# Performance work log

Measured on AMD Instinct MI355X. Metric: run time of the kernel, lower is better.

Reference implementation:

```python
import jax, jax.numpy as jnp
import numpy as np
import math

D_MODEL = 512
N_HEADS = 8
D_K = D_MODEL // N_HEADS
B, N = 2, 2048


def setup_inputs() -> dict:
    key = jax.random.key(0)
    ks = jax.random.split(key, 13)
    s = 1.0 / math.sqrt(D_MODEL)
    inp = {
        "x": jax.random.normal(ks[0], (B, N, D_MODEL), dtype=jnp.float32),
        "D": jax.random.uniform(ks[1], (B, N, N), dtype=jnp.float32),
        "A": jax.random.uniform(ks[2], (B, N, N), dtype=jnp.float32),
        "Wq": jax.random.normal(ks[3], (D_MODEL, D_MODEL), dtype=jnp.float32) * s,
        "bq": jnp.zeros((D_MODEL,), dtype=jnp.float32),
        "Wk": jax.random.normal(ks[4], (D_MODEL, D_MODEL), dtype=jnp.float32) * s,
        "bk": jnp.zeros((D_MODEL,), dtype=jnp.float32),
        "Wv": jax.random.normal(ks[5], (D_MODEL, D_MODEL), dtype=jnp.float32) * s,
        "bv": jnp.zeros((D_MODEL,), dtype=jnp.float32),
        "Wo": jax.random.normal(ks[6], (D_MODEL, D_MODEL), dtype=jnp.float32) * s,
        "bo": jnp.zeros((D_MODEL,), dtype=jnp.float32),
        # learned per-head bias scalars; init nonzero so biases matter numerically
        "w_d": jax.random.normal(ks[7], (1, N_HEADS, 1, 1), dtype=jnp.float32) * 0.1,
        "w_a": jax.random.normal(ks[8], (1, N_HEADS, 1, 1), dtype=jnp.float32) * 0.1,
    }
    return inp


def reference(x, D, A, Wq, bq, Wk, bk, Wv, bv, Wo, bo, w_d, w_a):
    b, n, _ = x.shape
    # project and split heads: (B, H, N, d_k)
    def heads(W, bias):
        return (x @ W.T + bias).reshape(b, n, N_HEADS, D_K).transpose(0, 2, 1, 3)
    q = heads(Wq, bq)
    k = heads(Wk, bk)
    v = heads(Wv, bv)
    scale = 1.0 / math.sqrt(D_K)
    # (B, H, N, N) scores with learned-scalar-weighted tree biases
    scores = jnp.einsum("bhqd,bhkd->bhqk", q, k) * scale
    scores = scores + w_d * D[:, None, :, :] + w_a * A[:, None, :, :]
    attn = jax.nn.softmax(scores, axis=-1)
    out = jnp.einsum("bhqk,bhkd->bhqd", attn, v)
    out = out.transpose(0, 2, 1, 3).reshape(b, n, D_MODEL)
    return out @ Wo.T + bo
```

## Files before the change

kernel.cpp:

```cpp
#include <hip/hip_runtime.h>
#include <hip/hip_bf16.h>
#include <math.h>

typedef unsigned short ushort_t;
typedef unsigned int   uint_t;
typedef __attribute__((ext_vector_type(8))) short  bf16x8;
typedef __attribute__((ext_vector_type(4))) float  f32x4;
typedef __attribute__((ext_vector_type(2))) int    i32x2;
typedef __attribute__((ext_vector_type(4))) short  s16x4;

#define MFMA16(a, b, c) __builtin_amdgcn_mfma_f32_16x16x32_bf16((a), (b), (c), 0, 0, 0)

static constexpr int BATCH = 2;
static constexpr int SEQ   = 2048;
static constexpr int DMODEL = 512;
static constexpr int NHEADS = 8;
static constexpr int DK    = 64;
static constexpr int MROWS = BATCH * SEQ;
static constexpr int XE = MROWS * DMODEL;
static constexpr int WE = DMODEL * DMODEL;
static constexpr int NQKV = 3 * DMODEL;
static constexpr int NSPLIT = 4;
static constexpr int KB_PER = (SEQ / 64) / NSPLIT;

static constexpr float QSCALE_L2E = 0.18033688011112043f;
static constexpr float L2E = 1.4426950408889634f;

__device__ __forceinline__ ushort_t f2bf(float f) {
  unsigned int u = __builtin_bit_cast(unsigned int, f);
  u = (u + 0x7FFFu + ((u >> 16) & 1u)) >> 16;
  return (ushort_t)u;
}

__device__ __forceinline__ float fexp2(float x) {
  float r;
  asm("v_exp_f32 %0, %1" : "=v"(r) : "v"(x));
  return r;
}

__device__ __forceinline__ int cvt_pk_bf16(float a, float b) {
  int r;
  asm("v_cvt_pk_bf16_f32 %0, %1, %2" : "=v"(r) : "v"(a), "v"(b));
  return r;
}

__device__ __forceinline__ float rowmax16(float x) {
  int t;
  t = __builtin_amdgcn_mov_dpp(__builtin_bit_cast(int, x), 0xB1, 0xF, 0xF, true);
  x = fmaxf(x, __builtin_bit_cast(float, t));
  t = __builtin_amdgcn_mov_dpp(__builtin_bit_cast(int, x), 0x4E, 0xF, 0xF, true);
  x = fmaxf(x, __builtin_bit_cast(float, t));
  t = __builtin_amdgcn_mov_dpp(__builtin_bit_cast(int, x), 0x141, 0xF, 0xF, true);
  x = fmaxf(x, __builtin_bit_cast(float, t));
  t = __builtin_amdgcn_mov_dpp(__builtin_bit_cast(int, x), 0x140, 0xF, 0xF, true);
  x = fmaxf(x, __builtin_bit_cast(float, t));
  return x;
}

__device__ __forceinline__ void async16(const ushort_t* g, ushort_t* l) {
  __builtin_amdgcn_global_load_lds(
      (const __attribute__((address_space(1))) unsigned int*)g,
      (__attribute__((address_space(3))) unsigned int*)l, 16, 0, 0);
}

__global__ __launch_bounds__(256) void convert_kernel(
    const float* __restrict__ x,  const float* __restrict__ wq,
    const float* __restrict__ wk, const float* __restrict__ wv,
    const float* __restrict__ wo,
    const float* __restrict__ bq, const float* __restrict__ bk,
    const float* __restrict__ bv,
    ushort_t* __restrict__ dst, float* __restrict__ bqkv) {
  const int bid = blockIdx.x;
  if (bid == (XE + 4 * WE) / 1024) {
    for (int i = threadIdx.x; i < NQKV; i += 256) {
      bqkv[i] = (i < 512) ? bq[i] * QSCALE_L2E
              : (i < 1024) ? bk[i - 512] : bv[i - 1024];
    }
    return;
  }
  int e = (bid * 256 + threadIdx.x) * 4;
  const float* src;
  int off;
  float qs = 1.0f;
  if (e < XE)                { src = x;  off = e; }
  else if (e < XE + WE)      { src = wq; off = e - XE; qs = QSCALE_L2E; }
  else if (e < XE + 2 * WE)  { src = wk; off = e - XE - WE; }
  else if (e < XE + 3 * WE)  { src = wv; off = e - XE - 2 * WE; }
  else                       { src = wo; off = e - XE - 3 * WE; }
  float4 f = *reinterpret_cast<const float4*>(&src[off]);
  s16x4 v;
  v[0] = (short)f2bf(f.x * qs); v[1] = (short)f2bf(f.y * qs);
  v[2] = (short)f2bf(f.z * qs); v[3] = (short)f2bf(f.w * qs);
  *reinterpret_cast<s16x4*>(&dst[e]) = v;
}

template <bool F32OUT>
__global__ __launch_bounds__(256) void gemm_bt128(
    const ushort_t* __restrict__ A, const ushort_t* __restrict__ Bt,
    const float* __restrict__ bias, void* __restrict__ C,
    int N, int K) {
  __shared__ ushort_t As[128][64];
  __shared__ ushort_t Bs[128][64];
  const int tid  = threadIdx.x;
  const int wave = tid >> 6, lane = tid & 63;
  const int quad = lane >> 4, l15 = lane & 15;
  const int m0 = blockIdx.y * 128, n0 = blockIdx.x * 128;
  const int wr = (wave >> 1) * 64, wc = (wave & 1) * 64;

  f32x4 acc[4][4] = {};

  const int lrow = lane >> 3, slot = lane & 7;
  const int cswz = 8 * (slot ^ lrow);
  const ushort_t* ag = A  + (size_t)(m0 + wave * 8 + lrow) * K + cswz;
  const ushort_t* bg = Bt + (size_t)(n0 + wave * 8 + lrow) * K + cswz;
  ushort_t* la[4]; ushort_t* lb[4];
#pragma unroll
  for (int r0 = 0; r0 < 4; r0++) {
    la[r0] = &As[r0 * 32 + wave * 8][0];
    lb[r0] = &Bs[r0 * 32 + wave * 8][0];
  }

  const int swz = l15 & 7;

  for (int k0 = 0; k0 < K; k0 += 64) {
    __syncthreads();
#pragma unroll
    for (int r0 = 0; r0 < 4; r0++)
      async16(ag + k0 + (size_t)(r0 * 32) * K, la[r0]);
#pragma unroll
    for (int r0 = 0; r0 < 4; r0++)
      async16(bg + k0 + (size_t)(r0 * 32) * K, lb[r0]);
    asm volatile("s_waitcnt vmcnt(0)" ::: "memory");
    __syncthreads();
#pragma unroll
    for (int s = 0; s < 2; s++) {
      const int acol = 8 * ((s * 4 + quad) ^ swz);
      bf16x8 af[4], bfr[4];
#pragma unroll
      for (int i = 0; i < 4; i++)
        af[i] = *reinterpret_cast<const bf16x8*>(&As[wr + i * 16 + l15][acol]);
#pragma unroll
      for (int j = 0; j < 4; j++)
        bfr[j] = *reinterpret_cast<const bf16x8*>(&Bs[wc + j * 16 + l15][acol]);
#pragma unroll
      for (int i = 0; i < 4; i++)
#pragma unroll
        for (int j = 0; j < 4; j++)
          acc[i][j] = MFMA16(af[i], bfr[j], acc[i][j]);
    }
  }

#pragma unroll
  for (int j = 0; j < 4; j++) {
    const int col = n0 + wc + j * 16 + l15;
    const float bv = bias[col];
#pragma unroll
    for (int i = 0; i < 4; i++) {
#pragma unroll
      for (int rr = 0; rr < 4; rr++) {
        const int row = m0 + wr + i * 16 + quad * 4 + rr;
        const float v = acc[i][j][rr] + bv;
        if (F32OUT) reinterpret_cast<float*>(C)[(size_t)row * N + col] = v;
        else        reinterpret_cast<ushort_t*>(C)[(size_t)row * N + col] = f2bf(v);
      }
    }
  }
}

__global__ __launch_bounds__(256) void attn_kernel(
    const ushort_t* __restrict__ QKV,
    const float* __restrict__ Dm, const float* __restrict__ Am,
    const float* __restrict__ wd, const float* __restrict__ wa,
    float* __restrict__ Opart, float* __restrict__ Mp, float* __restrict__ Lp) {
  const int qb = blockIdx.x, h = blockIdx.y;
  const int b = blockIdx.z / NSPLIT, split = blockIdx.z % NSPLIT;
  const int tid = threadIdx.x;
  const int wave = tid >> 6, lane = tid & 63;
  const int quad = lane >> 4, l15 = lane & 15;
  const int q0 = qb * 64;
  const float wdh = wd[h] * L2E, wah = wa[h] * L2E;

  __shared__ ushort_t Ks[64][64];
  __shared__ ushort_t Vts[64][64];
  __shared__ __align__(16) ushort_t Ps[4][16][72];

  const int qrow = q0 + wave * 16 + l15;
  bf16x8 qf[2];
#pragma unroll
  for (int s = 0; s < 2; s++)
    qf[s] = *reinterpret_cast<const bf16x8*>(
        &QKV[(size_t)(b * SEQ + qrow) * NQKV + h * DK + s * 32 + quad * 8]);

  bf16x8 ones;
#pragma unroll
  for (int j = 0; j < 8; j++) ones[j] = (short)0x3F80;

  float m_run[4], l_run[4];
  f32x4 o[4] = {};
#pragma unroll
  for (int rr = 0; rr < 4; rr++) { m_run[rr] = -INFINITY; l_run[rr] = 0.f; }

  const int lrow = lane >> 3, slot = lane & 7;
  const ushort_t* kg = QKV + (size_t)(b * SEQ + wave * 16 + lrow) * NQKV +
                       512 + h * DK + 8 * (slot ^ lrow);
  ushort_t* lk0 = &Ks[wave * 16][0];
  ushort_t* lk1 = &Ks[wave * 16 + 8][0];

  const int u  = tid >> 3;
  const int c7 = tid & 7;
  const int sc = c7 * 8;
  const int kv = ((u & 3) << 4) | (u >> 2);
  const ushort_t* vg = QKV + (size_t)(b * SEQ + kv) * NQKV + 1024 + h * DK + sc;
  const int col0 = (u & 7) + 8 * ((u >> 3) ^ c7);
  const int col1 = (u & 7) + 8 * (((u >> 3) + 4) ^ c7);

  const int swz = l15 & 7;

  const float* dD[4];
  const float* dA[4];
#pragma unroll
  for (int rr = 0; rr < 4; rr++) {
    const size_t rowoff = (size_t)b * SEQ * SEQ +
        (size_t)(q0 + wave * 16 + quad * 4 + rr) * SEQ + (size_t)split * KB_PER * 64 + l15;
    dD[rr] = Dm + rowoff;
    dA[rr] = Am + rowoff;
  }

  for (int kbi = 0; kbi < KB_PER; kbi++) {
    const int k0 = (split * KB_PER + kbi) * 64;
    __syncthreads();
    async16(kg + (size_t)k0 * NQKV, lk0);
    async16(kg + (size_t)(k0 + 8) * NQKV, lk1);
    bf16x8 v0 = *reinterpret_cast<const bf16x8*>(vg + (size_t)k0 * NQKV);
    bf16x8 v1 = *reinterpret_cast<const bf16x8*>(vg + (size_t)(k0 + 8) * NQKV);

    float dv[4][4], av[4][4];
#pragma unroll
    for (int t = 0; t < 4; t++) {
#pragma unroll
      for (int rr = 0; rr < 4; rr++) {
        dv[t][rr] = dD[rr][t * 16];
        av[t][rr] = dA[rr][t * 16];
      }
    }
#pragma unroll
    for (int rr = 0; rr < 4; rr++) { dD[rr] += 64; dA[rr] += 64; }

#pragma unroll
    for (int j = 0; j < 8; j++) {
      Vts[sc + j][col0] = (ushort_t)v0[j];
      Vts[sc + j][col1] = (ushort_t)v1[j];
    }
    asm volatile("s_waitcnt vmcnt(0)" ::: "memory");
    __syncthreads();

    f32x4 sacc[4];
#pragma unroll
    for (int t = 0; t < 4; t++) {
      bf16x8 kf0 = *reinterpret_cast<const bf16x8*>(&Ks[t * 16 + l15][8 * (quad ^ swz)]);
      bf16x8 kf1 = *reinterpret_cast<const bf16x8*>(&Ks[t * 16 + l15][8 * ((4 + quad) ^ swz)]);
      f32x4 z = {};
      z = MFMA16(qf[0], kf0, z);
      sacc[t] = MFMA16(qf[1], kf1, z);
    }

    float sv[4][4];
    float mx[4] = {-INFINITY, -INFINITY, -INFINITY, -INFINITY};
#pragma unroll
    for (int t = 0; t < 4; t++) {
#pragma unroll
      for (int rr = 0; rr < 4; rr++) {
        float s = fmaf(wdh, dv[t][rr], fmaf(wah, av[t][rr], sacc[t][rr]));
        sv[t][rr] = s;
        mx[rr] = fmaxf(mx[rr], s);
      }
    }
#pragma unroll
    for (int rr = 0; rr < 4; rr++) mx[rr] = rowmax16(mx[rr]);

    bool grow = false;
#pragma unroll
    for (int rr = 0; rr < 4; rr++) grow |= (mx[rr] > m_run[rr] + 11.5f);
    if (__ballot(grow)) {
      float alpha[4];
#pragma unroll
      for (int rr = 0; rr < 4; rr++) {
        const float mn = fmaxf(m_run[rr], mx[rr]);
        alpha[rr] = fexp2(m_run[rr] - mn);
        m_run[rr] = mn;
        l_run[rr] *= alpha[rr];
      }
#pragma unroll
      for (int dt = 0; dt < 4; dt++)
#pragma unroll
        for (int rr = 0; rr < 4; rr++) o[dt][rr] *= alpha[rr];
    }

#pragma unroll
    for (int rr = 0; rr < 4; rr++) {
      const float m = m_run[rr];
      i32x2 w;
      w[0] = cvt_pk_bf16(fexp2(sv[0][rr] - m), fexp2(sv[1][rr] - m));
      w[1] = cvt_pk_bf16(fexp2(sv[2][rr] - m), fexp2(sv[3][rr] - m));
      *reinterpret_cast<i32x2*>(&Ps[wave][quad * 4 + rr][l15 * 4]) = w;
    }

    asm volatile("s_waitcnt lgkmcnt(0)" ::: "memory");

    f32x4 rsacc = {};
#pragma unroll
    for (int s2 = 0; s2 < 2; s2++) {
      bf16x8 pf = *reinterpret_cast<const bf16x8*>(&Ps[wave][l15][s2 * 32 + quad * 8]);
#pragma unroll
      for (int dt = 0; dt < 4; dt++) {
        const int vrow = dt * 16 + l15;
        const int vcb = (s2 * 4 + quad) ^ (vrow >> 3);
        bf16x8 vf = *reinterpret_cast<const bf16x8*>(&Vts[vrow][vcb * 8]);
        o[dt] = MFMA16(pf, vf, o[dt]);
      }
      rsacc = MFMA16(pf, ones, rsacc);
    }
#pragma unroll
    for (int rr = 0; rr < 4; rr++) l_run[rr] += rsacc[rr];
  }

  const int pidx = (((b * NHEADS + h) * 32 + qb) * NSPLIT + split);
  float* op = Opart + (size_t)pidx * 4096;
#pragma unroll
  for (int dt = 0; dt < 4; dt++) {
#pragma unroll
    for (int rr = 0; rr < 4; rr++) {
      const int row = wave * 16 + quad * 4 + rr;
      op[row * 64 + dt * 16 + l15] = o[dt][rr];
    }
  }
  if (l15 == 0) {
#pragma unroll
    for (int rr = 0; rr < 4; rr++) {
      const int row = wave * 16 + quad * 4 + rr;
      Mp[(size_t)pidx * 64 + row] = m_run[rr];
      Lp[(size_t)pidx * 64 + row] = l_run[rr];
    }
  }
}

__global__ __launch_bounds__(256) void combine_kernel(
    const float* __restrict__ Opart, const float* __restrict__ Mp,
    const float* __restrict__ Lp, ushort_t* __restrict__ AO) {
  const int qb = blockIdx.x, h = blockIdx.y, b = blockIdx.z;
  const int tid = threadIdx.x;
  const int lane = tid & 63, wq = tid >> 6;
  const int pidx0 = ((b * NHEADS + h) * 32 + qb) * NSPLIT;

  for (int r = 0; r < 16; r++) {
    const int q = wq * 16 + r;
    float m[NSPLIT], l[NSPLIT];
    float M = -INFINITY;
#pragma unroll
    for (int s = 0; s < NSPLIT; s++) {
      m[s] = Mp[(size_t)(pidx0 + s) * 64 + q];
      l[s] = Lp[(size_t)(pidx0 + s) * 64 + q];
      M = fmaxf(M, m[s]);
    }
    float L = 0.f, acc = 0.f;
#pragma unroll
    for (int s = 0; s < NSPLIT; s++) {
      const float w = fexp2(m[s] - M);
      L += l[s] * w;
      acc += Opart[(size_t)(pidx0 + s) * 4096 + q * 64 + lane] * w;
    }
    const int row = b * SEQ + qb * 64 + q;
    AO[(size_t)row * DMODEL + h * DK + lane] = f2bf(acc / L);
  }
}

extern "C" void kernel_launch(void* const* d_in, const int* in_sizes, int n_in,
                              void* d_out, int out_size, void* d_ws, size_t ws_size,
                              hipStream_t stream) {
  const float* x  = (const float*)d_in[0];
  const float* Dm = (const float*)d_in[1];
  const float* Am = (const float*)d_in[2];
  const float* Wq = (const float*)d_in[3];
  const float* bq = (const float*)d_in[4];
  const float* Wk = (const float*)d_in[5];
  const float* bk = (const float*)d_in[6];
  const float* Wv = (const float*)d_in[7];
  const float* bv = (const float*)d_in[8];
  const float* Wo = (const float*)d_in[9];
  const float* bo = (const float*)d_in[10];
  const float* wd = (const float*)d_in[11];
  const float* wa = (const float*)d_in[12];

  char* ws = (char*)d_ws;
  size_t off = 0;
  ushort_t* xb    = (ushort_t*)(ws + off); off += (size_t)XE * 2;
  ushort_t* wqkvb = (ushort_t*)(ws + off); off += (size_t)3 * WE * 2;
  ushort_t* wob   = (ushort_t*)(ws + off); off += (size_t)WE * 2;
  ushort_t* QKVb  = (ushort_t*)(ws + off); off += (size_t)MROWS * NQKV * 2;
  ushort_t* AO    = (ushort_t*)(ws + off); off += (size_t)XE * 2;
  float*    bqkv  = (float*)(ws + off);    off += (size_t)NQKV * 4;
  off = (off + 255) & ~(size_t)255;
  float*    Opart = (float*)(ws + off);    off += (size_t)512 * NSPLIT * 4096 * 4;
  float*    Mpart = (float*)(ws + off);    off += (size_t)512 * NSPLIT * 64 * 4;
  float*    Lpart = (float*)(ws + off);

  const int conv_blocks = (XE + 4 * WE) / 1024;
  convert_kernel<<<conv_blocks + 1, 256, 0, stream>>>(
      x, Wq, Wk, Wv, Wo, bq, bk, bv, xb, bqkv);

  dim3 qkvgrid(NQKV / 128, MROWS / 128);
  gemm_bt128<false><<<qkvgrid, 256, 0, stream>>>(xb, wqkvb, bqkv, QKVb, NQKV, DMODEL);

  dim3 agrid(SEQ / 64, NHEADS, BATCH * NSPLIT);
  attn_kernel<<<agrid, 256, 0, stream>>>(QKVb, Dm, Am, wd, wa, Opart, Mpart, Lpart);
  dim3 cgrid(SEQ / 64, NHEADS, BATCH);
  combine_kernel<<<cgrid, 256, 0, stream>>>(Opart, Mpart, Lpart, AO);

  dim3 ogrid(DMODEL / 128, MROWS / 128);
  gemm_bt128<true><<<ogrid, 256, 0, stream>>>(AO, wob, bo, (float*)d_out, DMODEL, DMODEL);
}
```

Baseline: 221.1 us.

## Double-buffer K/V tiles and prefetch bias loads in attention loop

```diff
diff --git a/kernel.cpp b/kernel.cpp
--- a/kernel.cpp
+++ b/kernel.cpp
@@ -180,8 +180,8 @@
   const int q0 = qb * 64;
   const float wdh = wd[h] * L2E, wah = wa[h] * L2E;
 
-  __shared__ ushort_t Ks[64][64];
-  __shared__ ushort_t Vts[64][64];
+  __shared__ ushort_t Ks[2][64][64];
+  __shared__ ushort_t Vts[2][64][64];
   __shared__ __align__(16) ushort_t Ps[4][16][72];
 
   const int qrow = q0 + wave * 16 + l15;
@@ -203,8 +203,8 @@
   const int lrow = lane >> 3, slot = lane & 7;
   const ushort_t* kg = QKV + (size_t)(b * SEQ + wave * 16 + lrow) * NQKV +
                        512 + h * DK + 8 * (slot ^ lrow);
-  ushort_t* lk0 = &Ks[wave * 16][0];
-  ushort_t* lk1 = &Ks[wave * 16 + 8][0];
+  ushort_t* lk0[2] = {&Ks[0][wave * 16][0], &Ks[1][wave * 16][0]};
+  ushort_t* lk1[2] = {&Ks[0][wave * 16 + 8][0], &Ks[1][wave * 16 + 8][0]};
 
   const int u  = tid >> 3;
   const int c7 = tid & 7;
@@ -226,39 +226,38 @@
     dA[rr] = Am + rowoff;
   }
 
-  for (int kbi = 0; kbi < KB_PER; kbi++) {
-    const int k0 = (split * KB_PER + kbi) * 64;
-    __syncthreads();
-    async16(kg + (size_t)k0 * NQKV, lk0);
-    async16(kg + (size_t)(k0 + 8) * NQKV, lk1);
-    bf16x8 v0 = *reinterpret_cast<const bf16x8*>(vg + (size_t)k0 * NQKV);
-    bf16x8 v1 = *reinterpret_cast<const bf16x8*>(vg + (size_t)(k0 + 8) * NQKV);
-
-    float dv[4][4], av[4][4];
+  auto stage = [&](int tile, int bu, bf16x8& sv0, bf16x8& sv1,
+                   float (&sdv)[4][4], float (&sav)[4][4]) {
+    const int k0 = (split * KB_PER + tile) * 64;
+    async16(kg + (size_t)k0 * NQKV, lk0[bu]);
+    async16(kg + (size_t)(k0 + 8) * NQKV, lk1[bu]);
+    sv0 = *reinterpret_cast<const bf16x8*>(vg + (size_t)k0 * NQKV);
+    sv1 = *reinterpret_cast<const bf16x8*>(vg + (size_t)(k0 + 8) * NQKV);
+    const int c0 = tile * 64;
 #pragma unroll
     for (int t = 0; t < 4; t++) {
 #pragma unroll
       for (int rr = 0; rr < 4; rr++) {
-        dv[t][rr] = dD[rr][t * 16];
-        av[t][rr] = dA[rr][t * 16];
+        sdv[t][rr] = dD[rr][c0 + t * 16];
+        sav[t][rr] = dA[rr][c0 + t * 16];
       }
     }
-#pragma unroll
-    for (int rr = 0; rr < 4; rr++) { dD[rr] += 64; dA[rr] += 64; }
-
+  };
+
+  auto vwrite = [&](int bu, const bf16x8& v0, const bf16x8& v1) {
 #pragma unroll
     for (int j = 0; j < 8; j++) {
-      Vts[sc + j][col0] = (ushort_t)v0[j];
-      Vts[sc + j][col1] = (ushort_t)v1[j];
-    }
-    asm volatile("s_waitcnt vmcnt(0)" ::: "memory");
-    __syncthreads();
-
+      Vts[bu][sc + j][col0] = (ushort_t)v0[j];
+      Vts[bu][sc + j][col1] = (ushort_t)v1[j];
+    }
+  };
+
+  auto compute = [&](int bu, const float (&dv)[4][4], const float (&av)[4][4]) {
     f32x4 sacc[4];
 #pragma unroll
     for (int t = 0; t < 4; t++) {
-      bf16x8 kf0 = *reinterpret_cast<const bf16x8*>(&Ks[t * 16 + l15][8 * (quad ^ swz)]);
-      bf16x8 kf1 = *reinterpret_cast<const bf16x8*>(&Ks[t * 16 + l15][8 * ((4 + quad) ^ swz)]);
+      bf16x8 kf0 = *reinterpret_cast<const bf16x8*>(&Ks[bu][t * 16 + l15][8 * (quad ^ swz)]);
+      bf16x8 kf1 = *reinterpret_cast<const bf16x8*>(&Ks[bu][t * 16 + l15][8 * ((4 + quad) ^ swz)]);
       f32x4 z = {};
       z = MFMA16(qf[0], kf0, z);
       sacc[t] = MFMA16(qf[1], kf1, z);
@@ -315,13 +314,31 @@
       for (int dt = 0; dt < 4; dt++) {
         const int vrow = dt * 16 + l15;
         const int vcb = (s2 * 4 + quad) ^ (vrow >> 3);
-        bf16x8 vf = *reinterpret_cast<const bf16x8*>(&Vts[vrow][vcb * 8]);
+        bf16x8 vf = *reinterpret_cast<const bf16x8*>(&Vts[bu][vrow][vcb * 8]);
         o[dt] = MFMA16(pf, vf, o[dt]);
       }
       rsacc = MFMA16(pf, ones, rsacc);
     }
 #pragma unroll
     for (int rr = 0; rr < 4; rr++) l_run[rr] += rsacc[rr];
+  };
+
+  bf16x8 vA0, vA1, vB0, vB1;
+  float dvA[4][4], avA[4][4], dvB[4][4], avB[4][4];
+  stage(0, 0, vA0, vA1, dvA, avA);
+
+  for (int kbi = 0; kbi < KB_PER; kbi += 2) {
+    asm volatile("s_waitcnt vmcnt(0)" ::: "memory");
+    vwrite(0, vA0, vA1);
+    __syncthreads();
+    stage(kbi + 1, 1, vB0, vB1, dvB, avB);
+    compute(0, dvA, avA);
+
+    asm volatile("s_waitcnt vmcnt(0)" ::: "memory");
+    vwrite(1, vB0, vB1);
+    __syncthreads();
+    if (kbi + 2 < KB_PER) stage(kbi + 2, 0, vA0, vA1, dvA, avA);
+    compute(1, dvB, avB);
   }
 
   const int pidx = (((b * NHEADS + h) * 32 + qb) * NSPLIT + split);
```

After: 233.2 us. +5.5%, slower.
